# Kernel optimization log

Hardware: AMD Instinct MI355X
Metric: run time of the kernel (lower is better)

## Reference

```python
import jax, jax.numpy as jnp
import numpy as np

DIM = 384
HEADS = 8
EPS = 1e-5


def _layernorm(x, g, b):
    mu = jnp.mean(x, axis=-1, keepdims=True)
    var = jnp.mean(jnp.square(x - mu), axis=-1, keepdims=True)
    return (x - mu) * jax.lax.rsqrt(var + EPS) * g + b


def setup_inputs() -> dict:
    key = jax.random.key(0)
    ks = jax.random.split(key, 16)
    d = DIM
    s = lambda k, shape, scale=0.02: jax.random.normal(k, shape, dtype=jnp.float32) * scale
    return {
        "x": jax.random.normal(ks[0], (16, d, 32, 32), dtype=jnp.float32),
        "pos_w": s(ks[1], (d, 1, 3, 3), 0.1),   # depthwise conv kernel (OIHW, I=1)
        "pos_b": jnp.zeros((d,), jnp.float32),
        "g1": jnp.ones((d,), jnp.float32),
        "b1": jnp.zeros((d,), jnp.float32),
        "wqkv": s(ks[2], (d, 3 * d)),
        "bqkv": jnp.zeros((3 * d,), jnp.float32),
        "wproj": s(ks[3], (d, d)),
        "bproj": jnp.zeros((d,), jnp.float32),
        "g2": jnp.ones((d,), jnp.float32),
        "b2": jnp.zeros((d,), jnp.float32),
        "w1": s(ks[4], (d, 4 * d)),
        "bf1": jnp.zeros((4 * d,), jnp.float32),
        "w2": s(ks[5], (4 * d, d)),
        "bf2": jnp.zeros((d,), jnp.float32),
    }


def reference(x, pos_w, pos_b, g1, b1, wqkv, bqkv, wproj, bproj, g2, b2, w1, bf1, w2, bf2):
    B, C, H, W = x.shape
    # depthwise 3x3 conv positional embedding, residual
    pe = jax.lax.conv_general_dilated(
        x, pos_w, window_strides=(1, 1), padding=((1, 1), (1, 1)),
        dimension_numbers=("NCHW", "OIHW", "NCHW"), feature_group_count=C)
    x = x + pe + pos_b[None, :, None, None]
    # to tokens [B, N, C]
    t = x.reshape(B, C, H * W).transpose(0, 2, 1)
    N = H * W
    Dh = C // HEADS
    # attention
    xn = _layernorm(t, g1, b1)
    qkv = xn @ wqkv + bqkv                                   # [B,N,3C]
    qkv = qkv.reshape(B, N, 3, HEADS, Dh)
    q, k, v = qkv[:, :, 0], qkv[:, :, 1], qkv[:, :, 2]        # [B,N,H,Dh]
    scale = Dh ** -0.5
    attn = jnp.einsum("bqhd,bkhd->bhqk", q, k) * scale
    attn = jax.nn.softmax(attn, axis=-1)
    o = jnp.einsum("bhqk,bkhd->bqhd", attn, v).reshape(B, N, C)
    t = t + o @ wproj + bproj
    # MLP
    yn = _layernorm(t, g2, b2)
    h = jax.nn.gelu(yn @ w1 + bf1, approximate=False)
    t = t + h @ w2 + bf2
    return t.transpose(0, 2, 1).reshape(B, C, H, W)
```

## Files before the change

### kernel.cpp

```cpp
#include <hip/hip_runtime.h>
#include <hip/hip_bf16.h>
#include <math.h>

#define BATCH 16
#define CDIM 384
#define HH 32
#define WW 32
#define NPIX 1024
#define MTOK (BATCH * NPIX)
#define NHEADS 8
#define DH 48
#define QKVN (3 * CDIM)
#define FFN (4 * CDIM)

typedef unsigned short u16;
typedef unsigned int u32;
typedef __attribute__((ext_vector_type(8))) short short8;
typedef __attribute__((ext_vector_type(4))) float floatx4;

#define MFMA16(a, b, c) __builtin_amdgcn_mfma_f32_16x16x32_bf16(a, b, c, 0, 0, 0)

__device__ __forceinline__ void gl2lds16(const void* g, void* l) {
    __builtin_amdgcn_global_load_lds(
        (const __attribute__((address_space(1))) void*)g,
        (__attribute__((address_space(3))) void*)l, 16, 0, 0);
}

__global__ __launch_bounds__(256) void conv_pe_kernel(const float* __restrict__ x,
                                                      const float* __restrict__ pos_w,
                                                      const float* __restrict__ pos_b,
                                                      float* __restrict__ t) {
    __shared__ float xs[64][100];
    __shared__ float os[32][68];
    const int cg = blockIdx.x, h = blockIdx.y, b = blockIdx.z;
    const int tid = threadIdx.x;
    const int c0 = cg * 64;

#pragma unroll
    for (int it = 0; it < 6; ++it) {
        int task = tid + it * 256;
        int c = task / 24, rem = task % 24;
        int row = rem >> 3, f4 = rem & 7;
        int hh = h + row - 1;
        float4 v = {0.f, 0.f, 0.f, 0.f};
        if (hh >= 0 && hh < HH)
            v = *(const float4*)(x + (((size_t)(b * CDIM + c0 + c) * HH + hh) * WW + f4 * 4));
        *(float4*)&xs[c][row * 32 + f4 * 4] = v;
    }
    __syncthreads();

    const int c = tid >> 2, w0 = (tid & 3) * 8;
    float wgt[9];
#pragma unroll
    for (int i = 0; i < 9; ++i) wgt[i] = pos_w[(c0 + c) * 9 + i];
    const float pb = pos_b[c0 + c];
#pragma unroll
    for (int wi = 0; wi < 8; ++wi) {
        int w = w0 + wi;
        float acc = 0.f;
#pragma unroll
        for (int r = 0; r < 3; ++r)
#pragma unroll
            for (int kw = 0; kw < 3; ++kw) {
                int w2 = w + kw - 1;
                if (w2 >= 0 && w2 < WW) acc += xs[c][r * 32 + w2] * wgt[r * 3 + kw];
            }
        os[w][c] = xs[c][32 + w] + acc + pb;
    }
    __syncthreads();

    float* dstb = t + (size_t)(b * NPIX + h * 32) * CDIM + c0;
#pragma unroll
    for (int it = 0; it < 2; ++it) {
        int task = tid + it * 256;
        int px = task >> 4, f4 = task & 15;
        *(float4*)(dstb + (size_t)px * CDIM + f4 * 4) = *(const float4*)&os[px][f4 * 4];
    }
}

__global__ void ln_kernel(const float* __restrict__ in,
                          const float* __restrict__ g,
                          const float* __restrict__ bta,
                          __hip_bfloat16* __restrict__ out) {
    int m = blockIdx.x;
    const float* row = in + (size_t)m * CDIM;
    int tid = threadIdx.x;
    float v0 = row[tid], v1 = row[tid + 128], v2 = row[tid + 256];
    float s = v0 + v1 + v2;
    float ss = v0 * v0 + v1 * v1 + v2 * v2;
#pragma unroll
    for (int off = 32; off > 0; off >>= 1) {
        s += __shfl_down(s, off, 64);
        ss += __shfl_down(ss, off, 64);
    }
    __shared__ float red[4];
    if ((tid & 63) == 0) { red[tid >> 6] = s; red[2 + (tid >> 6)] = ss; }
    __syncthreads();
    float sum = red[0] + red[1], sumsq = red[2] + red[3];
    float mu = sum * (1.f / CDIM);
    float var = sumsq * (1.f / CDIM) - mu * mu;
    float rstd = rsqrtf(var + 1e-5f);
    __hip_bfloat16* orow = out + (size_t)m * CDIM;
    orow[tid]       = __float2bfloat16((v0 - mu) * rstd * g[tid] + bta[tid]);
    orow[tid + 128] = __float2bfloat16((v1 - mu) * rstd * g[tid + 128] + bta[tid + 128]);
    orow[tid + 256] = __float2bfloat16((v2 - mu) * rstd * g[tid + 256] + bta[tid + 256]);
}

__global__ void wt_kernel(const float* __restrict__ W, __hip_bfloat16* __restrict__ Wt,
                          int K, int N) {
    __shared__ float tile[32][33];
    int n0 = blockIdx.x * 32, k0 = blockIdx.y * 32;
    int tx = threadIdx.x & 31, ty = threadIdx.x >> 5;
    for (int i = ty; i < 32; i += 8) tile[i][tx] = W[(size_t)(k0 + i) * N + n0 + tx];
    __syncthreads();
    for (int i = ty; i < 32; i += 8)
        Wt[(size_t)(n0 + i) * K + k0 + tx] = __float2bfloat16(tile[tx][i]);
}

__global__ __launch_bounds__(256) void vtrans_kernel(const u16* __restrict__ qkv,
                                                     u16* __restrict__ vT) {
    __shared__ u16 Vl[48][136];
    const int kt = blockIdx.x, h = blockIdx.y, b = blockIdx.z;
    const int tid = threadIdx.x;
    const size_t base = (size_t)b * NPIX * QKVN + 2 * CDIM + (size_t)h * DH;
#pragma unroll
    for (int it = 0; it < 3; ++it) {
        int task = tid + it * 256;
        int key = task / 6, ch = task - key * 6;
        short8 v = *(const short8*)(qkv + base + (size_t)(kt * 128 + key) * QKVN + ch * 8);
#pragma unroll
        for (int i = 0; i < 8; ++i) Vl[ch * 8 + i][key] = (u16)v[i];
    }
    __syncthreads();
    u16* dst = vT + (size_t)(b * NHEADS + h) * DH * NPIX + (size_t)kt * 128;
#pragma unroll
    for (int it = 0; it < 3; ++it) {
        int task = tid + it * 256;
        int d = task >> 4, ch = task & 15;
        short8 v = *(const short8*)&Vl[d][ch * 8];
        *(short8*)(dst + (size_t)d * NPIX + ch * 8) = v;
    }
}

template <int BN, int BK, int RES, int ACT, int OUTBF>
__global__ __launch_bounds__(256) void gemm_bf16(
    const u16* __restrict__ A, const u16* __restrict__ Bt,
    const float* __restrict__ bias, const float* __restrict__ Res,
    void* __restrict__ Cout, int N, int K) {
    constexpr int KC = BK / 32;
    constexpr int NF = BN / 32;
    __shared__ u16 As[2][KC][128 * 32];
    __shared__ u16 Bs[2][KC][BN * 32];
    const int tid = threadIdx.x;
    const int lane = tid & 63;
    const int wv = tid >> 6;
    const int qd = lane >> 4;
    const int l16 = lane & 15;
    const int wy = wv >> 1, wx = wv & 1;

    const int id = blockIdx.x;
    const int xcd = id & 7, j = id >> 3;
    const int m0 = (xcd * 16 + (j & 15)) * 128;
    const int n0 = (j >> 4) * BN;

    const int rr = tid >> 2, cc = (tid & 3) * 8;
    const u16* Ag = A + (size_t)(m0 + rr) * K + cc;
    const u16* Bg = Bt + (size_t)(n0 + rr) * K + cc;

    const floatx4 fz = {0.f, 0.f, 0.f, 0.f};
    floatx4 acc[4][NF];
#pragma unroll
    for (int i = 0; i < 4; ++i)
#pragma unroll
        for (int jj = 0; jj < NF; ++jj) acc[i][jj] = fz;

    auto stage = [&](int slot, int k0) {
#pragma unroll
        for (int kc = 0; kc < KC; ++kc) {
            gl2lds16(Ag + k0 + kc * 32, &As[slot][kc][0] + tid * 8);
            gl2lds16(Ag + (size_t)64 * K + k0 + kc * 32, &As[slot][kc][0] + 2048 + tid * 8);
            gl2lds16(Bg + k0 + kc * 32, &Bs[slot][kc][0] + tid * 8);
            if (NF == 4) gl2lds16(Bg + (size_t)64 * K + k0 + kc * 32, &Bs[slot][kc][0] + 2048 + tid * 8);
        }
    };

    stage(0, 0);
    const int iters = K / BK;
    for (int it = 0; it < iters; ++it) {
        const int slot = it & 1;
        __syncthreads();
        if (it + 1 < iters) stage(slot ^ 1, (it + 1) * BK);
#pragma unroll
        for (int kc = 0; kc < KC; ++kc) {
            short8 af[4], bfr[NF];
#pragma unroll
            for (int i = 0; i < 4; ++i)
                af[i] = *(const short8*)(&As[slot][kc][0] + (wy * 64 + i * 16 + l16) * 32 + qd * 8);
#pragma unroll
            for (int jj = 0; jj < NF; ++jj)
                bfr[jj] = *(const short8*)(&Bs[slot][kc][0] + (wx * (BN / 2) + jj * 16 + l16) * 32 + qd * 8);
#pragma unroll
            for (int i = 0; i < 4; ++i)
#pragma unroll
                for (int jj = 0; jj < NF; ++jj) acc[i][jj] = MFMA16(af[i], bfr[jj], acc[i][jj]);
        }
    }

    const int colb = n0 + wx * (BN / 2) + l16;
    const int rowb = m0 + wy * 64 + qd * 4;
#pragma unroll
    for (int jj = 0; jj < NF; ++jj) {
        int col = colb + jj * 16;
        float bb = bias[col];
#pragma unroll
        for (int i = 0; i < 4; ++i) {
            int row = rowb + i * 16;
#pragma unroll
            for (int r = 0; r < 4; ++r) {
                float c = acc[i][jj][r] + bb;
                if (RES) c += Res[(size_t)(row + r) * N + col];
                if (ACT) c = 0.5f * c * (1.f + erff(c * 0.70710678118654752f));
                if (OUTBF)
                    ((__hip_bfloat16*)Cout)[(size_t)(row + r) * N + col] = __float2bfloat16(c);
                else
                    ((float*)Cout)[(size_t)(row + r) * N + col] = c;
            }
        }
    }
}

__global__ __launch_bounds__(256) void attn_kernel(const u16* __restrict__ qkv,
                                                   const u16* __restrict__ vT,
                                                   __hip_bfloat16* __restrict__ ob) {
    const int id = blockIdx.x;
    const int h = id & 7;
    const int b = (id >> 3) & 15;
    const int qb = id >> 7;
    const int tid = threadIdx.x;
    const int lane = tid & 63, wv = tid >> 6;
    const int qd = lane >> 4, l16 = lane & 15;

    __shared__ u16 Kl[2][65][48];
    __shared__ u16 Vt[48][72];
    __shared__ __hip_bfloat16 Pl[4][32][72];

    if (tid < 24) { ((u32*)&Kl[0][64][0])[tid] = 0; ((u32*)&Kl[1][64][0])[tid] = 0; }

    const size_t bh = (size_t)b * NPIX * QKVN + (size_t)h * DH;
    const u16* vtb = vT + (size_t)(b * NHEADS + h) * DH * NPIX;

    auto stageK = [&](int kt, int slot) {
        const size_t kbase = bh + (size_t)(kt * 64) * QKVN + CDIM;
        int key = tid / 6, ch = tid - key * 6;
        gl2lds16(qkv + kbase + (size_t)key * QKVN + ch * 8, &Kl[slot][0][0] + tid * 8);
        if (tid < 128) {
            int t2 = tid + 256;
            int k2 = t2 / 6, c2 = t2 - k2 * 6;
            gl2lds16(qkv + kbase + (size_t)k2 * QKVN + c2 * 8, &Kl[slot][0][0] + t2 * 8);
        }
    };
    const int vd = tid >> 3, vc = tid & 7, vd1 = (tid + 256) >> 3;
    short8 vA, vB;
    auto loadV = [&](int kt) {
        vA = *(const short8*)(vtb + (size_t)vd * NPIX + kt * 64 + vc * 8);
        if (tid < 128) vB = *(const short8*)(vtb + (size_t)vd1 * NPIX + kt * 64 + vc * 8);
    };

    short8 qf[2][2];
    const short8 z8 = {0, 0, 0, 0, 0, 0, 0, 0};
#pragma unroll
    for (int g = 0; g < 2; ++g) {
        const u16* gq = qkv + bh + (size_t)(qb * 128 + wv * 32 + g * 16 + l16) * QKVN;
        qf[g][0] = *(const short8*)(gq + qd * 8);
        qf[g][1] = (qd < 2) ? *(const short8*)(gq + 32 + qd * 8) : z8;
    }

    const floatx4 fz = {0.f, 0.f, 0.f, 0.f};
    floatx4 o[2][3];
    float lsum[2][4];
#pragma unroll
    for (int g = 0; g < 2; ++g) {
#pragma unroll
        for (int nt = 0; nt < 3; ++nt) o[g][nt] = fz;
#pragma unroll
        for (int r = 0; r < 4; ++r) lsum[g][r] = 0.f;
    }
    const float scale = 0.14433756729740643f;

    stageK(0, 0);
    loadV(0);

    for (int kt = 0; kt < 16; ++kt) {
        const int cur = kt & 1;
        __syncthreads();
        *(short8*)&Vt[vd][vc * 8] = vA;
        if (tid < 128) *(short8*)&Vt[vd1][vc * 8] = vB;
        __syncthreads();
        if (kt + 1 < 16) { stageK(kt + 1, cur ^ 1); loadV(kt + 1); }

        short8 kl[4], kh[4];
#pragma unroll
        for (int t = 0; t < 4; ++t) {
            const u16* kr = &Kl[cur][0][0] + (t * 16 + l16) * 48;
            kl[t] = *(const short8*)(kr + qd * 8);
            kh[t] = *(const short8*)(kr + 32 + qd * 8);
        }
        floatx4 s[2][4];
#pragma unroll
        for (int g = 0; g < 2; ++g)
#pragma unroll
            for (int t = 0; t < 4; ++t) {
                floatx4 a = fz;
                a = MFMA16(qf[g][0], kl[t], a);
                a = MFMA16(qf[g][1], kh[t], a);
                s[g][t] = a;
            }

#pragma unroll
        for (int g = 0; g < 2; ++g)
#pragma unroll
            for (int t = 0; t < 4; ++t) {
#pragma unroll
                for (int r = 0; r < 4; ++r) {
                    float p = __expf(s[g][t][r] * scale);
                    Pl[wv][g * 16 + qd * 4 + r][t * 16 + l16] = __float2bfloat16(p);
                    lsum[g][r] += p;
                }
            }

        short8 vl[3], vh[3];
#pragma unroll
        for (int nt = 0; nt < 3; ++nt) {
            const u16* vr = &Vt[0][0] + (nt * 16 + l16) * 72;
            vl[nt] = *(const short8*)(vr + qd * 8);
            vh[nt] = *(const short8*)(vr + 32 + qd * 8);
        }
#pragma unroll
        for (int g = 0; g < 2; ++g) {
            const __hip_bfloat16* prr = &Pl[wv][g * 16 + l16][0];
            short8 ap0 = *(const short8*)(prr + qd * 8);
            short8 ap1 = *(const short8*)(prr + 32 + qd * 8);
#pragma unroll
            for (int nt = 0; nt < 3; ++nt) {
                o[g][nt] = MFMA16(ap0, vl[nt], o[g][nt]);
                o[g][nt] = MFMA16(ap1, vh[nt], o[g][nt]);
            }
        }
    }

#pragma unroll
    for (int g = 0; g < 2; ++g)
#pragma unroll
        for (int r = 0; r < 4; ++r) {
            float l = lsum[g][r];
            l += __shfl_xor(l, 1, 64);
            l += __shfl_xor(l, 2, 64);
            l += __shfl_xor(l, 4, 64);
            l += __shfl_xor(l, 8, 64);
            float inv = 1.f / l;
            size_t row = (size_t)(b * NPIX + qb * 128 + wv * 32 + g * 16 + qd * 4 + r) * CDIM + h * DH;
#pragma unroll
            for (int nt = 0; nt < 3; ++nt)
                ob[row + nt * 16 + l16] = __float2bfloat16(o[g][nt][r] * inv);
        }
}

__global__ void transpose_kernel(const float* __restrict__ t, float* __restrict__ out) {
    __shared__ float tile[32][33];
    int b = blockIdx.z;
    int n0 = blockIdx.x * 32;
    int c0 = blockIdx.y * 32;
    int tx = threadIdx.x & 31;
    int ty = threadIdx.x >> 5;
    for (int i = ty; i < 32; i += 8)
        tile[i][tx] = t[(size_t)(b * NPIX + n0 + i) * CDIM + c0 + tx];
    __syncthreads();
    int c = threadIdx.x >> 3, f4 = threadIdx.x & 7;
    float4 v;
    v.x = tile[f4 * 4 + 0][c];
    v.y = tile[f4 * 4 + 1][c];
    v.z = tile[f4 * 4 + 2][c];
    v.w = tile[f4 * 4 + 3][c];
    *(float4*)(out + (size_t)(b * CDIM + c0 + c) * NPIX + n0 + f4 * 4) = v;
}

extern "C" void kernel_launch(void* const* d_in, const int* in_sizes, int n_in,
                              void* d_out, int out_size, void* d_ws, size_t ws_size,
                              hipStream_t stream) {
    const float* x = (const float*)d_in[0];
    const float* pos_w = (const float*)d_in[1];
    const float* pos_b = (const float*)d_in[2];
    const float* g1 = (const float*)d_in[3];
    const float* b1 = (const float*)d_in[4];
    const float* wqkv = (const float*)d_in[5];
    const float* bqkv = (const float*)d_in[6];
    const float* wproj = (const float*)d_in[7];
    const float* bproj = (const float*)d_in[8];
    const float* g2 = (const float*)d_in[9];
    const float* b2 = (const float*)d_in[10];
    const float* w1 = (const float*)d_in[11];
    const float* bf1 = (const float*)d_in[12];
    const float* w2 = (const float*)d_in[13];
    const float* bf2 = (const float*)d_in[14];
    float* out = (float*)d_out;

    char* ws = (char*)d_ws;
    float* t = (float*)ws;
    __hip_bfloat16* xn = (__hip_bfloat16*)(ws + 25165824);
    u16* vTb = (u16*)xn;
    __hip_bfloat16* wqkvT = (__hip_bfloat16*)(ws + 37748736);
    __hip_bfloat16* wprojT = (__hip_bfloat16*)(ws + 38633472);
    __hip_bfloat16* w1T = (__hip_bfloat16*)(ws + 38928384);
    __hip_bfloat16* w2T = (__hip_bfloat16*)(ws + 40108032);
    char* big = ws + 41287680;
    u16* qkvb = (u16*)big;
    __hip_bfloat16* obb = (__hip_bfloat16*)(big + 37748736);
    u16* hb = (u16*)big;

    wt_kernel<<<dim3(QKVN / 32, CDIM / 32), 256, 0, stream>>>(wqkv, wqkvT, CDIM, QKVN);
    wt_kernel<<<dim3(CDIM / 32, CDIM / 32), 256, 0, stream>>>(wproj, wprojT, CDIM, CDIM);
    wt_kernel<<<dim3(FFN / 32, CDIM / 32), 256, 0, stream>>>(w1, w1T, CDIM, FFN);
    wt_kernel<<<dim3(CDIM / 32, FFN / 32), 256, 0, stream>>>(w2, w2T, FFN, CDIM);

    conv_pe_kernel<<<dim3(CDIM / 64, HH, BATCH), 256, 0, stream>>>(x, pos_w, pos_b, t);
    ln_kernel<<<MTOK, 128, 0, stream>>>(t, g1, b1, xn);
    gemm_bf16<128, 32, 0, 0, 1><<<dim3(128 * (QKVN / 128)), 256, 0, stream>>>(
        (const u16*)xn, (const u16*)wqkvT, bqkv, nullptr, qkvb, QKVN, CDIM);
    vtrans_kernel<<<dim3(NPIX / 128, NHEADS, BATCH), 256, 0, stream>>>(qkvb, vTb);
    attn_kernel<<<dim3(1024), 256, 0, stream>>>(qkvb, vTb, obb);
    gemm_bf16<64, 64, 1, 0, 0><<<dim3(128 * (CDIM / 64)), 256, 0, stream>>>(
        (const u16*)obb, (const u16*)wprojT, bproj, t, t, CDIM, CDIM);
    ln_kernel<<<MTOK, 128, 0, stream>>>(t, g2, b2, xn);
    gemm_bf16<128, 32, 0, 1, 1><<<dim3(128 * (FFN / 128)), 256, 0, stream>>>(
        (const u16*)xn, (const u16*)w1T, bf1, nullptr, hb, FFN, CDIM);
    gemm_bf16<64, 64, 1, 0, 0><<<dim3(128 * (CDIM / 64)), 256, 0, stream>>>(
        (const u16*)hb, (const u16*)w2T, bf2, t, t, CDIM, FFN);
    transpose_kernel<<<dim3(32, 12, BATCH), 256, 0, stream>>>(t, out);
}
```

Baseline: 341.2 us.

## Swap MFMA operand order for row-contiguous vector epilogues and streamlined attention softmax

The GEMM swaps the A/B operands of the MFMA so each lane holds four consecutive columns of one row. The epilogue can then load bias and residual as float4 and store packed bf16 or float4 vectors instead of scalar strided stores. In attention, Q is pre-scaled by scale*log2e so exp2 can be used, and S^T is computed so each lane owns one query row. P is written to LDS as packed vectors, the per-row sum reduction shrinks, and the output is stored vectorized. The new bf16 packing rounds half-up rather than round-to-nearest-even, and pre-scaling Q in bf16 adds slight precision loss.

Result: no change. 340.0 us (-0.3%).

```diff
diff --git a/kernel.cpp b/kernel.cpp
--- a/kernel.cpp
+++ b/kernel.cpp
@@ -24,6 +24,17 @@
     __builtin_amdgcn_global_load_lds(
         (const __attribute__((address_space(1))) void*)g,
         (__attribute__((address_space(3))) void*)l, 16, 0, 0);
+}
+
+__device__ __forceinline__ u32 pkbf(float a, float b) {
+    u32 ua = __float_as_uint(a) + 0x8000u;
+    u32 ub = __float_as_uint(b) + 0x8000u;
+    return __builtin_amdgcn_perm(ub, ua, 0x07060302u);
+}
+__device__ __forceinline__ float bf2f(u16 h) { return __uint_as_float(((u32)h) << 16); }
+__device__ __forceinline__ u16 f2bf(float f) {
+    u32 u = __float_as_uint(f);
+    return (u16)((u + 0x7FFFu + ((u >> 16) & 1u)) >> 16);
 }
 
 __global__ __launch_bounds__(256) void conv_pe_kernel(const float* __restrict__ x,
@@ -202,28 +213,39 @@
 #pragma unroll
             for (int i = 0; i < 4; ++i)
 #pragma unroll
-                for (int jj = 0; jj < NF; ++jj) acc[i][jj] = MFMA16(af[i], bfr[jj], acc[i][jj]);
-        }
-    }
-
-    const int colb = n0 + wx * (BN / 2) + l16;
-    const int rowb = m0 + wy * 64 + qd * 4;
+                for (int jj = 0; jj < NF; ++jj) acc[i][jj] = MFMA16(bfr[jj], af[i], acc[i][jj]);
+        }
+    }
+
+    const int rowb = m0 + wy * 64 + l16;
+    const int colb = n0 + wx * (BN / 2) + qd * 4;
 #pragma unroll
     for (int jj = 0; jj < NF; ++jj) {
         int col = colb + jj * 16;
-        float bb = bias[col];
+        float4 bb = *(const float4*)(bias + col);
 #pragma unroll
         for (int i = 0; i < 4; ++i) {
             int row = rowb + i * 16;
-#pragma unroll
-            for (int r = 0; r < 4; ++r) {
-                float c = acc[i][jj][r] + bb;
-                if (RES) c += Res[(size_t)(row + r) * N + col];
-                if (ACT) c = 0.5f * c * (1.f + erff(c * 0.70710678118654752f));
-                if (OUTBF)
-                    ((__hip_bfloat16*)Cout)[(size_t)(row + r) * N + col] = __float2bfloat16(c);
-                else
-                    ((float*)Cout)[(size_t)(row + r) * N + col] = c;
+            floatx4 a = acc[i][jj];
+            float v0 = a[0] + bb.x, v1 = a[1] + bb.y, v2 = a[2] + bb.z, v3 = a[3] + bb.w;
+            if (RES) {
+                float4 rv = *(const float4*)(Res + (size_t)row * N + col);
+                v0 += rv.x; v1 += rv.y; v2 += rv.z; v3 += rv.w;
+            }
+            if (ACT) {
+                v0 = 0.5f * v0 * (1.f + erff(v0 * 0.70710678118654752f));
+                v1 = 0.5f * v1 * (1.f + erff(v1 * 0.70710678118654752f));
+                v2 = 0.5f * v2 * (1.f + erff(v2 * 0.70710678118654752f));
+                v3 = 0.5f * v3 * (1.f + erff(v3 * 0.70710678118654752f));
+            }
+            if (OUTBF) {
+                uint2 pk;
+                pk.x = pkbf(v0, v1);
+                pk.y = pkbf(v2, v3);
+                *(uint2*)((__hip_bfloat16*)Cout + (size_t)row * N + col) = pk;
+            } else {
+                float4 st = {v0, v1, v2, v3};
+                *(float4*)((float*)Cout + (size_t)row * N + col) = st;
             }
         }
     }
@@ -241,8 +263,8 @@
     const int qd = lane >> 4, l16 = lane & 15;
 
     __shared__ u16 Kl[2][65][48];
-    __shared__ u16 Vt[48][72];
-    __shared__ __hip_bfloat16 Pl[4][32][72];
+    __shared__ __align__(16) u16 Vt[48][72];
+    __shared__ __align__(16) u16 Plt[4][16][72];
 
     if (tid < 24) { ((u32*)&Kl[0][64][0])[tid] = 0; ((u32*)&Kl[1][64][0])[tid] = 0; }
 
@@ -266,26 +288,30 @@
         if (tid < 128) vB = *(const short8*)(vtb + (size_t)vd1 * NPIX + kt * 64 + vc * 8);
     };
 
+    const float qsc = 0.14433756729740643f * 1.4426950408889634f;
     short8 qf[2][2];
     const short8 z8 = {0, 0, 0, 0, 0, 0, 0, 0};
 #pragma unroll
     for (int g = 0; g < 2; ++g) {
         const u16* gq = qkv + bh + (size_t)(qb * 128 + wv * 32 + g * 16 + l16) * QKVN;
-        qf[g][0] = *(const short8*)(gq + qd * 8);
-        qf[g][1] = (qd < 2) ? *(const short8*)(gq + 32 + qd * 8) : z8;
+        short8 q0 = *(const short8*)(gq + qd * 8);
+        short8 q1 = (qd < 2) ? *(const short8*)(gq + 32 + qd * 8) : z8;
+#pragma unroll
+        for (int e = 0; e < 8; ++e) {
+            q0[e] = (short)f2bf(bf2f((u16)q0[e]) * qsc);
+            q1[e] = (short)f2bf(bf2f((u16)q1[e]) * qsc);
+        }
+        qf[g][0] = q0;
+        qf[g][1] = q1;
     }
 
     const floatx4 fz = {0.f, 0.f, 0.f, 0.f};
     floatx4 o[2][3];
-    float lsum[2][4];
-#pragma unroll
-    for (int g = 0; g < 2; ++g) {
+    float lsum[2] = {0.f, 0.f};
+#pragma unroll
+    for (int g = 0; g < 2; ++g)
 #pragma unroll
         for (int nt = 0; nt < 3; ++nt) o[g][nt] = fz;
-#pragma unroll
-        for (int r = 0; r < 4; ++r) lsum[g][r] = 0.f;
-    }
-    const float scale = 0.14433756729740643f;
 
     stageK(0, 0);
     loadV(0);
@@ -305,29 +331,6 @@
             kl[t] = *(const short8*)(kr + qd * 8);
             kh[t] = *(const short8*)(kr + 32 + qd * 8);
         }
-        floatx4 s[2][4];
-#pragma unroll
-        for (int g = 0; g < 2; ++g)
-#pragma unroll
-            for (int t = 0; t < 4; ++t) {
-                floatx4 a = fz;
-                a = MFMA16(qf[g][0], kl[t], a);
-                a = MFMA16(qf[g][1], kh[t], a);
-                s[g][t] = a;
-            }
-
-#pragma unroll
-        for (int g = 0; g < 2; ++g)
-#pragma unroll
-            for (int t = 0; t < 4; ++t) {
-#pragma unroll
-                for (int r = 0; r < 4; ++r) {
-                    float p = __expf(s[g][t][r] * scale);
-                    Pl[wv][g * 16 + qd * 4 + r][t * 16 + l16] = __float2bfloat16(p);
-                    lsum[g][r] += p;
-                }
-            }
-
         short8 vl[3], vh[3];
 #pragma unroll
         for (int nt = 0; nt < 3; ++nt) {
@@ -335,34 +338,52 @@
             vl[nt] = *(const short8*)(vr + qd * 8);
             vh[nt] = *(const short8*)(vr + 32 + qd * 8);
         }
+
 #pragma unroll
         for (int g = 0; g < 2; ++g) {
-            const __hip_bfloat16* prr = &Pl[wv][g * 16 + l16][0];
-            short8 ap0 = *(const short8*)(prr + qd * 8);
-            short8 ap1 = *(const short8*)(prr + 32 + qd * 8);
+#pragma unroll
+            for (int t = 0; t < 4; ++t) {
+                floatx4 a = fz;
+                a = MFMA16(kl[t], qf[g][0], a);
+                a = MFMA16(kh[t], qf[g][1], a);
+                float p0 = __builtin_amdgcn_exp2f(a[0]);
+                float p1 = __builtin_amdgcn_exp2f(a[1]);
+                float p2 = __builtin_amdgcn_exp2f(a[2]);
+                float p3 = __builtin_amdgcn_exp2f(a[3]);
+                lsum[g] += (p0 + p1) + (p2 + p3);
+                uint2 w;
+                w.x = pkbf(p0, p1);
+                w.y = pkbf(p2, p3);
+                *(uint2*)&Plt[wv][l16][t * 16 + qd * 4] = w;
+            }
+            short8 ap0 = *(const short8*)&Plt[wv][l16][qd * 8];
+            short8 ap1 = *(const short8*)&Plt[wv][l16][32 + qd * 8];
 #pragma unroll
             for (int nt = 0; nt < 3; ++nt) {
-                o[g][nt] = MFMA16(ap0, vl[nt], o[g][nt]);
-                o[g][nt] = MFMA16(ap1, vh[nt], o[g][nt]);
-            }
-        }
-    }
-
-#pragma unroll
-    for (int g = 0; g < 2; ++g)
-#pragma unroll
-        for (int r = 0; r < 4; ++r) {
-            float l = lsum[g][r];
-            l += __shfl_xor(l, 1, 64);
-            l += __shfl_xor(l, 2, 64);
-            l += __shfl_xor(l, 4, 64);
-            l += __shfl_xor(l, 8, 64);
-            float inv = 1.f / l;
-            size_t row = (size_t)(b * NPIX + qb * 128 + wv * 32 + g * 16 + qd * 4 + r) * CDIM + h * DH;
-#pragma unroll
-            for (int nt = 0; nt < 3; ++nt)
-                ob[row + nt * 16 + l16] = __float2bfloat16(o[g][nt][r] * inv);
-        }
+                o[g][nt] = MFMA16(vl[nt], ap0, o[g][nt]);
+                o[g][nt] = MFMA16(vh[nt], ap1, o[g][nt]);
+            }
+        }
+    }
+
+#pragma unroll
+    for (int g = 0; g < 2; ++g) {
+        float l = lsum[g];
+        l += __shfl_xor(l, 16, 64);
+        l += __shfl_xor(l, 32, 64);
+        float inv = 1.f / l;
+        __hip_bfloat16* orow =
+            ob + (size_t)(b * NPIX + qb * 128 + wv * 32 + g * 16 + l16) * CDIM + h * DH;
+#pragma unroll
+        for (int nt = 0; nt < 3; ++nt) {
+            float v0 = o[g][nt][0] * inv, v1 = o[g][nt][1] * inv;
+            float v2 = o[g][nt][2] * inv, v3 = o[g][nt][3] * inv;
+            uint2 w;
+            w.x = pkbf(v0, v1);
+            w.y = pkbf(v2, v3);
+            *(uint2*)(orow + nt * 16 + qd * 4) = w;
+        }
+    }
 }
 
 __global__ void transpose_kernel(const float* __restrict__ t, float* __restrict__ out) {
```
